# Kernel optimization log

Measured on AMD Instinct MI355X. Metric: run time of the kernel, lower is better.

## Reference

```python
import jax, jax.numpy as jnp
import numpy as np

B, T, D, H, F = 8, 1024, 512, 8, 2048
DK = D // H
EPS = 1e-3  # Keras LayerNormalization default epsilon
NEG = -1e9


def layer_norm(x, g, b):
    mu = jnp.mean(x, axis=-1, keepdims=True)
    var = jnp.mean(jnp.square(x - mu), axis=-1, keepdims=True)
    return (x - mu) * jax.lax.rsqrt(var + EPS) * g + b


def setup_inputs() -> dict:
    key = jax.random.key(0)
    ks = jax.random.split(key, 16)
    s = 1.0 / np.sqrt(D)
    sf = 1.0 / np.sqrt(F)
    x = jax.random.normal(ks[0], (B, T, D), dtype=jnp.float32)
    # binary attention mask (1 = attend). Random block-sparse-ish pattern.
    mask = (jax.random.uniform(ks[1], (B, 1, T, T)) > 0.15).astype(jnp.float32)
    return {
        "x": x,
        "mask": mask,
        "ln_in_g": jnp.ones((D,), jnp.float32),
        "ln_in_b": jnp.zeros((D,), jnp.float32),
        "Wq": jax.random.normal(ks[2], (D, D), jnp.float32) * s,
        "bq": jnp.zeros((D,), jnp.float32),
        "Wk": jax.random.normal(ks[3], (D, D), jnp.float32) * s,
        "bk": jnp.zeros((D,), jnp.float32),
        "Wv": jax.random.normal(ks[4], (D, D), jnp.float32) * s,
        "bv": jnp.zeros((D,), jnp.float32),
        "ln1_g": jnp.ones((D,), jnp.float32),
        "ln1_b": jnp.zeros((D,), jnp.float32),
        "W1": jax.random.normal(ks[5], (D, F), jnp.float32) * s,
        "b1": jnp.zeros((F,), jnp.float32),
        "W2": jax.random.normal(ks[6], (F, D), jnp.float32) * sf,
        "b2": jnp.zeros((D,), jnp.float32),
        "ln2_g": jnp.ones((D,), jnp.float32),
        "ln2_b": jnp.zeros((D,), jnp.float32),
    }


def reference(x, mask, ln_in_g, ln_in_b, Wq, bq, Wk, bk, Wv, bv,
              ln1_g, ln1_b, W1, b1, W2, b2, ln2_g, ln2_b):
    bs = x.shape[0]
    h = layer_norm(x, ln_in_g, ln_in_b)                      # [B,T,D]
    # QKV projections, split heads -> [B,H,T,DK]
    q = (h @ Wq + bq).reshape(bs, -1, H, DK).transpose(0, 2, 1, 3)
    k = (h @ Wk + bk).reshape(bs, -1, H, DK).transpose(0, 2, 1, 3)
    v = (h @ Wv + bv).reshape(bs, -1, H, DK).transpose(0, 2, 1, 3)
    scores = jnp.einsum('bhtd,bhsd->bhts', q, k) / np.sqrt(DK)
    scores = scores + NEG * (1.0 - mask)                     # additive mask
    probs = jax.nn.softmax(scores, axis=-1)                  # dropout: identity at inference
    attn = jnp.einsum('bhts,bhsd->bhtd', probs, v)
    attn = attn.transpose(0, 2, 1, 3).reshape(bs, -1, H * DK)
    # residual with ORIGINAL inputs (pre-ln_in), as in call() -> attend(inputs,...)
    attn = attn + x
    a = layer_norm(attn, ln1_g, ln1_b)
    f = jax.nn.relu(a @ W1 + b1) @ W2 + b2
    out = layer_norm(f + a, ln2_g, ln2_b)
    return out
```

## Files before the change

### kernel.cpp

```cpp
#include <hip/hip_runtime.h>

typedef unsigned short u16;
typedef unsigned long long u64;
typedef __bf16 bf16x8 __attribute__((ext_vector_type(8)));
typedef float f32x4 __attribute__((ext_vector_type(4)));

#define B_ 8
#define T_ 1024
#define D_ 512
#define H_ 8
#define DK_ 64
#define F_ 2048

__device__ __forceinline__ u16 f2bf(float f) {
    unsigned u = __float_as_uint(f);
    u += 0x7fffu + ((u >> 16) & 1u);
    return (u16)(u >> 16);
}
__device__ __forceinline__ float bf2f(u16 v) {
    return __uint_as_float((unsigned)v << 16);
}

__device__ __forceinline__ void tile_transcvt(
    const float* __restrict__ W, u16* __restrict__ WT, int K, int N, int k0, int n0,
    u16 (*t)[72])
{
    const int tid = threadIdx.x;
    const int r = tid >> 2, c4 = (tid & 3) * 16;
    const float* src = W + (size_t)(k0 + r) * N + n0 + c4;
#pragma unroll
    for (int j = 0; j < 16; j += 4) {
        float4 v = *(const float4*)(src + j);
        t[r][c4 + j]     = f2bf(v.x);
        t[r][c4 + j + 1] = f2bf(v.y);
        t[r][c4 + j + 2] = f2bf(v.z);
        t[r][c4 + j + 3] = f2bf(v.w);
    }
    __syncthreads();
    u16 tmp[16];
#pragma unroll
    for (int j = 0; j < 16; ++j) tmp[j] = t[c4 + j][r];
    u16* dst = WT + (size_t)(n0 + r) * K + k0 + c4;
    *(uint4*)dst       = *(uint4*)&tmp[0];
    *(uint4*)(dst + 8) = *(uint4*)&tmp[8];
}

__global__ __launch_bounds__(256) void prep_all(
    const float* __restrict__ Wq, const float* __restrict__ Wk, const float* __restrict__ Wv,
    const float* __restrict__ bq, const float* __restrict__ bk, const float* __restrict__ bv,
    const float* __restrict__ W1, const float* __restrict__ W2,
    const float* __restrict__ mask,
    u16* __restrict__ WqkvT, u16* __restrict__ W1T, u16* __restrict__ W2T,
    float* __restrict__ bias, u64* __restrict__ Mb)
{
    __shared__ u16 t[64][72];
    const int blk = blockIdx.x;
    const int tid = threadIdx.x;
    if (blk < 192) {
        const int k0 = (blk & 7) * 64;
        const int n0 = (blk >> 3) * 64;
        const float* W = (n0 < 512) ? Wq : (n0 < 1024 ? Wk : Wv);
        if (k0 == 0 && tid < 64) {
            int n = n0 + tid;
            bias[n] = (n < 512) ? bq[n] : (n < 1024 ? bk[n - 512] : bv[n - 1024]);
        }
        const int r = tid >> 2, c4 = (tid & 3) * 16;
        const float* src = W + (size_t)(k0 + r) * 512 + (n0 & 511) + c4;
#pragma unroll
        for (int j = 0; j < 16; j += 4) {
            float4 v = *(const float4*)(src + j);
            t[r][c4 + j]     = f2bf(v.x);
            t[r][c4 + j + 1] = f2bf(v.y);
            t[r][c4 + j + 2] = f2bf(v.z);
            t[r][c4 + j + 3] = f2bf(v.w);
        }
        __syncthreads();
        u16 tmp[16];
#pragma unroll
        for (int j = 0; j < 16; ++j) tmp[j] = t[c4 + j][r];
        u16* dst = WqkvT + (size_t)(n0 + r) * 512 + k0 + c4;
        *(uint4*)dst       = *(uint4*)&tmp[0];
        *(uint4*)(dst + 8) = *(uint4*)&tmp[8];
    } else if (blk < 448) {
        const int idx = blk - 192;
        tile_transcvt(W1, W1T, 512, 2048, (idx & 7) * 64, (idx >> 3) * 64, t);
    } else if (blk < 704) {
        const int idx = blk - 448;
        tile_transcvt(W2, W2T, 2048, 512, (idx & 31) * 64, (idx >> 5) * 64, t);
    } else {
        const int idx = blk - 704;
        int gw = (idx * 256 + tid) >> 6;
        int lane = tid & 63;
#pragma unroll
        for (int i = 0; i < 16; ++i) {
            size_t chunk = (size_t)gw * 16 + i;
            float v = mask[chunk * 64 + lane];
            u64 bm = __ballot(v > 0.5f);
            if (lane == 0) Mb[chunk] = bm;
        }
    }
}

template<int XBF, int RBF, int OB, int OF, int FILL>
__global__ __launch_bounds__(256) void ln_t(
    const void* __restrict__ Xv, const void* __restrict__ Rv,
    const float* __restrict__ g, const float* __restrict__ bt,
    u16* __restrict__ ob, float* __restrict__ of,
    const float* __restrict__ fillsrc, float* __restrict__ filldst)
{
    int wave = threadIdx.x >> 6, lane = threadIdx.x & 63;
    int row = blockIdx.x * 4 + wave;
    size_t base = (size_t)row * D_ + lane * 8;
    int c0 = lane * 8;
    float v[8];
    if (XBF) {
        const u16* X = (const u16*)Xv;
        uint4 a = *(const uint4*)(X + base);
        u16 tu[8]; *(uint4*)tu = a;
#pragma unroll
        for (int j = 0; j < 8; ++j) v[j] = bf2f(tu[j]);
    } else {
        const float* X = (const float*)Xv;
        float4 a0 = *(const float4*)(X + base);
        float4 a1 = *(const float4*)(X + base + 4);
        v[0]=a0.x; v[1]=a0.y; v[2]=a0.z; v[3]=a0.w;
        v[4]=a1.x; v[5]=a1.y; v[6]=a1.z; v[7]=a1.w;
    }
    if (Rv) {
        if (RBF) {
            const u16* R = (const u16*)Rv;
            uint4 a = *(const uint4*)(R + base);
            u16 tu[8]; *(uint4*)tu = a;
#pragma unroll
            for (int j = 0; j < 8; ++j) v[j] += bf2f(tu[j]);
        } else {
            const float* R = (const float*)Rv;
            float4 r0 = *(const float4*)(R + base);
            float4 r1 = *(const float4*)(R + base + 4);
            v[0]+=r0.x; v[1]+=r0.y; v[2]+=r0.z; v[3]+=r0.w;
            v[4]+=r1.x; v[5]+=r1.y; v[6]+=r1.z; v[7]+=r1.w;
        }
    }
    if (FILL) {
        float4 f0 = *(const float4*)(fillsrc + c0);
        float4 f1v = *(const float4*)(fillsrc + c0 + 4);
        *(float4*)(filldst + base) = f0;
        *(float4*)(filldst + base + 4) = f1v;
    }
    float s = 0.f, q = 0.f;
#pragma unroll
    for (int j = 0; j < 8; ++j) { s += v[j]; q += v[j] * v[j]; }
#pragma unroll
    for (int off = 32; off > 0; off >>= 1) {
        s += __shfl_xor(s, off);
        q += __shfl_xor(q, off);
    }
    float mu = s * (1.0f / D_);
    float var = q * (1.0f / D_) - mu * mu;
    float rstd = rsqrtf(var + 1e-3f);
    float y[8];
#pragma unroll
    for (int j = 0; j < 8; ++j) y[j] = (v[j] - mu) * rstd * g[c0 + j] + bt[c0 + j];
    if (OB) {
        u16 t[8];
#pragma unroll
        for (int j = 0; j < 8; ++j) t[j] = f2bf(y[j]);
        *(uint4*)(ob + base) = *(uint4*)t;
    }
    if (OF) {
        float4 o0, o1;
        o0.x=y[0]; o0.y=y[1]; o0.z=y[2]; o0.w=y[3];
        o1.x=y[4]; o1.y=y[5]; o1.z=y[6]; o1.w=y[7];
        *(float4*)(of + base) = o0;
        *(float4*)(of + base + 4) = o1;
    }
}

template<int BN, int RELU, int OUT>
__global__ __launch_bounds__(256) void gemm_db(
    const u16* __restrict__ A, const u16* __restrict__ BT,
    const float* __restrict__ bias, u16* __restrict__ Cb,
    float* __restrict__ Cf, int N, int K, int KS)
{
    constexpr int NI = BN / 32;
    __shared__ u16 As[2][128 * 32];
    __shared__ u16 Bs[2][BN * 32];
    const int nb = gridDim.x;
    const int flat = blockIdx.y * nb + blockIdx.x;
    const int xcd = flat & 7;
    const int idx = flat >> 3;
    const int nblk = idx >> 3;
    const int mblk = xcd * 8 + (idx & 7);
    const int tid = threadIdx.x;
    const int wave = tid >> 6, lane = tid & 63;
    const int quad = lane >> 4, l16 = lane & 15;
    const int wr = wave >> 1, wc = wave & 1;
    const int rowBase = mblk * 128;
    const int colBase = nblk * BN;
    const int lr = lane >> 2;
    const int lc = (lane & 3) * 8;
    const int kOff = blockIdx.z * KS;
    const u16* Abase = A  + (size_t)(rowBase + lr) * K + kOff + lc;
    const u16* Bbase = BT + (size_t)(colBase + lr) * K + kOff + lc;

    auto stage = [&](int k0, int buf) {
#pragma unroll
        for (int c = 0; c < 2; ++c) {
            int chunk = wave * 2 + c;
            const u16* gp = Abase + (size_t)(chunk * 16) * K + k0;
            __builtin_amdgcn_global_load_lds(
                (const __attribute__((address_space(1))) unsigned int*)gp,
                (__attribute__((address_space(3))) unsigned int*)&As[buf][chunk * 512],
                16, 0, 0);
        }
#pragma unroll
        for (int c = 0; c < BN / 64; ++c) {
            int chunk = wave * (BN / 64) + c;
            const u16* gp = Bbase + (size_t)(chunk * 16) * K + k0;
            __builtin_amdgcn_global_load_lds(
                (const __attribute__((address_space(1))) unsigned int*)gp,
                (__attribute__((address_space(3))) unsigned int*)&Bs[buf][chunk * 512],
                16, 0, 0);
        }
    };

    f32x4 acc[4][NI] = {};
    stage(0, 0);
    for (int k0 = 0; k0 < KS; k0 += 32) {
        const int buf = (k0 >> 5) & 1;
        __syncthreads();
        if (k0 + 32 < KS) stage(k0 + 32, buf ^ 1);
        bf16x8 af[4], bfr[NI];
#pragma unroll
        for (int i = 0; i < 4; ++i)
            af[i] = *(const bf16x8*)&As[buf][(wr * 64 + i * 16 + l16) * 32 + quad * 8];
#pragma unroll
        for (int j = 0; j < NI; ++j)
            bfr[j] = *(const bf16x8*)&Bs[buf][(wc * (BN / 2) + j * 16 + l16) * 32 + quad * 8];
#pragma unroll
        for (int i = 0; i < 4; ++i)
#pragma unroll
            for (int j = 0; j < NI; ++j)
                acc[i][j] = __builtin_amdgcn_mfma_f32_16x16x32_bf16(af[i], bfr[j], acc[i][j], 0, 0, 0);
    }
#pragma unroll
    for (int i = 0; i < 4; ++i) {
        int row0 = rowBase + wr * 64 + i * 16 + quad * 4;
#pragma unroll
        for (int j = 0; j < NI; ++j) {
            int col = colBase + wc * (BN / 2) + j * 16 + l16;
            float bv = (OUT == 2) ? 0.0f : bias[col];
#pragma unroll
            for (int r = 0; r < 4; ++r) {
                float v = acc[i][j][r] + bv;
                if (RELU) v = fmaxf(v, 0.0f);
                if (OUT == 2)      atomicAdd(&Cf[(size_t)(row0 + r) * N + col], v);
                else if (OUT == 1) Cb[(size_t)(row0 + r) * N + col] = f2bf(v);
                else               Cf[(size_t)(row0 + r) * N + col] = v;
            }
        }
    }
}

__global__ __launch_bounds__(256) void vtrans(const u16* __restrict__ QKV, u16* __restrict__ Vt)
{
    int blk = blockIdx.x;
    int bh = blk >> 4;
    int t0 = (blk & 15) * 64;
    int b = bh >> 3, h = bh & 7;
    __shared__ u16 tile[64][72];
    int tid = threadIdx.x;
    int r = tid >> 2;
    int c = (tid & 3) * 16;
    const u16* src = QKV + ((size_t)(b * T_) + t0 + r) * (3 * D_) + 2 * D_ + h * DK_ + c;
    *(uint4*)&tile[r][c]     = *(const uint4*)(src);
    *(uint4*)&tile[r][c + 8] = *(const uint4*)(src + 8);
    __syncthreads();
    u16 tmp[16];
#pragma unroll
    for (int j = 0; j < 16; ++j) tmp[j] = tile[c + j][r];
    u16* dst = Vt + ((size_t)bh * DK_ + r) * T_ + t0 + c;
    *(uint4*)dst       = *(uint4*)&tmp[0];
    *(uint4*)(dst + 8) = *(uint4*)&tmp[8];
}

#define APAD 72
__global__ __launch_bounds__(256) void attn_kernel(
    const u16* __restrict__ QKV, const u16* __restrict__ Vt,
    const u64* __restrict__ Mb, u16* __restrict__ Out)
{
    const int flat = blockIdx.x + 16 * (blockIdx.y + 8 * blockIdx.z);
    const int xcd = flat & 7, slot = flat >> 3;
    const int bh = xcd * 8 + (slot >> 4);
    const int qt = slot & 15;
    const int b = bh >> 3, h = bh & 7;
    const int qBase = qt * 64;
    const int tid = threadIdx.x;
    const int wave = tid >> 6, lane = tid & 63;
    const int quad = lane >> 4, l16 = lane & 15;
    __shared__ u16 Ks[64][APAD];
    __shared__ u16 Vs[64][APAD];
    __shared__ u16 Ps[4][16][APAD];

    const int qRow = qBase + wave * 16 + l16;
    const u16* qptr = QKV + ((size_t)(b * T_) + qRow) * (3 * D_) + h * DK_;
    bf16x8 qf0 = *(const bf16x8*)(qptr + quad * 8);
    bf16x8 qf1 = *(const bf16x8*)(qptr + 32 + quad * 8);

    float l_i[4] = {0.f, 0.f, 0.f, 0.f};
    f32x4 o[4] = {{0,0,0,0},{0,0,0,0},{0,0,0,0},{0,0,0,0}};

    const int sr = tid >> 2;
    const int sc = (tid & 3) * 8;
    const u16* Kg = QKV + (size_t)(b * T_) * (3 * D_) + D_ + h * DK_;
    const u16* Vg = Vt + (size_t)(b * H_ + h) * DK_ * T_;
    const u64* Mg = Mb + ((size_t)(b * T_) + qBase + wave * 16 + quad * 4) * (T_ / 64);

    uint4 kb0 = *(const uint4*)(Kg + (size_t)sr * (3 * D_) + sc);
    uint4 kb1 = *(const uint4*)(Kg + (size_t)sr * (3 * D_) + sc + 32);
    uint4 vb0 = *(const uint4*)(Vg + (size_t)sr * T_ + sc);
    uint4 vb1 = *(const uint4*)(Vg + (size_t)sr * T_ + sc + 32);

    for (int s0 = 0; s0 < T_; s0 += 64) {
        __syncthreads();
        *(uint4*)&Ks[sr][sc]      = kb0;
        *(uint4*)&Ks[sr][sc + 32] = kb1;
        *(uint4*)&Vs[sr][sc]      = vb0;
        *(uint4*)&Vs[sr][sc + 32] = vb1;
        __syncthreads();
        if (s0 + 64 < T_) {
            int s1 = s0 + 64;
            kb0 = *(const uint4*)(Kg + (size_t)(s1 + sr) * (3 * D_) + sc);
            kb1 = *(const uint4*)(Kg + (size_t)(s1 + sr) * (3 * D_) + sc + 32);
            vb0 = *(const uint4*)(Vg + (size_t)sr * T_ + s1 + sc);
            vb1 = *(const uint4*)(Vg + (size_t)sr * T_ + s1 + sc + 32);
        }

        u64 m64[4];
#pragma unroll
        for (int r = 0; r < 4; ++r) m64[r] = Mg[(size_t)r * (T_ / 64) + (s0 >> 6)];

#pragma unroll
        for (int n = 0; n < 4; ++n) {
            f32x4 s4 = {0.f, 0.f, 0.f, 0.f};
            bf16x8 kf0 = *(const bf16x8*)&Ks[n * 16 + l16][quad * 8];
            bf16x8 kf1 = *(const bf16x8*)&Ks[n * 16 + l16][32 + quad * 8];
            s4 = __builtin_amdgcn_mfma_f32_16x16x32_bf16(qf0, kf0, s4, 0, 0, 0);
            s4 = __builtin_amdgcn_mfma_f32_16x16x32_bf16(qf1, kf1, s4, 0, 0, 0);
#pragma unroll
            for (int r = 0; r < 4; ++r) {
                float p = __expf(fmaf(s4[r], 0.125f, -10.0f));
                p = ((m64[r] >> (n * 16 + l16)) & 1ull) ? p : 0.0f;
                l_i[r] += p;
                Ps[wave][quad * 4 + r][n * 16 + l16] = f2bf(p);
            }
        }
        bf16x8 pf0 = *(const bf16x8*)&Ps[wave][l16][quad * 8];
        bf16x8 pf1 = *(const bf16x8*)&Ps[wave][l16][32 + quad * 8];
#pragma unroll
        for (int dt = 0; dt < 4; ++dt) {
            bf16x8 vf0 = *(const bf16x8*)&Vs[dt * 16 + l16][quad * 8];
            bf16x8 vf1 = *(const bf16x8*)&Vs[dt * 16 + l16][32 + quad * 8];
            o[dt] = __builtin_amdgcn_mfma_f32_16x16x32_bf16(pf0, vf0, o[dt], 0, 0, 0);
            o[dt] = __builtin_amdgcn_mfma_f32_16x16x32_bf16(pf1, vf1, o[dt], 0, 0, 0);
        }
    }
#pragma unroll
    for (int off = 1; off < 16; off <<= 1) {
#pragma unroll
        for (int r = 0; r < 4; ++r) l_i[r] += __shfl_xor(l_i[r], off);
    }
    float inv[4];
#pragma unroll
    for (int r = 0; r < 4; ++r) inv[r] = 1.0f / l_i[r];
    const int orow = qBase + wave * 16 + quad * 4;
    u16* Ob = Out + ((size_t)(b * T_) + orow) * D_ + h * DK_;
#pragma unroll
    for (int dt = 0; dt < 4; ++dt) {
#pragma unroll
        for (int r = 0; r < 4; ++r)
            Ob[(size_t)r * D_ + dt * 16 + l16] = f2bf(o[dt][r] * inv[r]);
    }
}

extern "C" void kernel_launch(void* const* d_in, const int* in_sizes, int n_in,
                              void* d_out, int out_size, void* d_ws, size_t ws_size,
                              hipStream_t stream)
{
    const float* x       = (const float*)d_in[0];
    const float* mask    = (const float*)d_in[1];
    const float* ln_in_g = (const float*)d_in[2];
    const float* ln_in_b = (const float*)d_in[3];
    const float* Wq      = (const float*)d_in[4];
    const float* bq      = (const float*)d_in[5];
    const float* Wk      = (const float*)d_in[6];
    const float* bk      = (const float*)d_in[7];
    const float* Wv      = (const float*)d_in[8];
    const float* bv      = (const float*)d_in[9];
    const float* ln1_g   = (const float*)d_in[10];
    const float* ln1_b   = (const float*)d_in[11];
    const float* W1      = (const float*)d_in[12];
    const float* b1      = (const float*)d_in[13];
    const float* W2      = (const float*)d_in[14];
    const float* b2      = (const float*)d_in[15];
    const float* ln2_g   = (const float*)d_in[16];
    const float* ln2_b   = (const float*)d_in[17];
    float* out = (float*)d_out;

    char* ws = (char*)d_ws;
    size_t off = 0;
    auto alloc = [&](size_t bytes) -> void* {
        void* p = ws + off;
        off = (off + bytes + 255) & ~(size_t)255;
        return p;
    };
    u16*   WqkvT   = (u16*)alloc((size_t)1536 * 512 * 2);
    u16*   W1T     = (u16*)alloc((size_t)2048 * 512 * 2);
    u16*   W2T     = (u16*)alloc((size_t)512 * 2048 * 2);
    float* bias_q  = (float*)alloc(1536 * 4);
    u64*   Mb      = (u64*)alloc((size_t)B_ * T_ * (T_ / 64) * 8);
    u16*   h_bf    = (u16*)alloc((size_t)8192 * 512 * 2);
    u16*   QKV     = (u16*)alloc((size_t)8192 * 1536 * 2);
    u16*   Vt      = (u16*)alloc((size_t)B_ * H_ * DK_ * T_ * 2);
    u16*   attn_bf = (u16*)alloc((size_t)8192 * 512 * 2);
    u16*   a_bf    = (u16*)alloc((size_t)8192 * 512 * 2);
    u16*   f1      = (u16*)alloc((size_t)8192 * 2048 * 2);
    float* f2      = (float*)alloc((size_t)8192 * 512 * 4);
    if (off > ws_size) return;

    prep_all<<<2752, 256, 0, stream>>>(Wq, Wk, Wv, bq, bk, bv, W1, W2, mask,
                                       WqkvT, W1T, W2T, bias_q, Mb);

    ln_t<0, 0, 1, 0, 0><<<2048, 256, 0, stream>>>(
        x, nullptr, ln_in_g, ln_in_b, h_bf, nullptr, nullptr, nullptr);

    gemm_db<128, 0, 1><<<dim3(12, 64, 1), 256, 0, stream>>>(
        h_bf, WqkvT, bias_q, QKV, nullptr, 1536, 512, 512);

    vtrans<<<1024, 256, 0, stream>>>(QKV, Vt);

    attn_kernel<<<dim3(16, 8, 8), 256, 0, stream>>>(QKV, Vt, Mb, attn_bf);

    ln_t<1, 0, 1, 0, 1><<<2048, 256, 0, stream>>>(
        attn_bf, x, ln1_g, ln1_b, a_bf, nullptr, b2, f2);

    gemm_db<128, 1, 1><<<dim3(16, 64, 1), 256, 0, stream>>>(
        a_bf, W1T, b1, f1, nullptr, 2048, 512, 512);

    gemm_db<64, 0, 2><<<dim3(8, 64, 2), 256, 0, stream>>>(
        f1, W2T, nullptr, nullptr, f2, 512, 2048, 1024);

    ln_t<0, 1, 0, 1, 0><<<2048, 256, 0, stream>>>(
        f2, a_bf, ln2_g, ln2_b, nullptr, out, nullptr, nullptr);
}
```

Measured before the change: 296.9 us.

## Shrink GEMM M-tile to 64 rows and drop split-K atomics for W2 GEMM

The GEMM kernel now uses 64-row M tiles instead of 128, doubling the number of blocks for every projection and FFN GEMM. The second FFN GEMM no longer splits K across two blocks with atomicAdd into a bias-prefilled buffer. It writes f32 output directly with the bias added in the epilogue, so the LayerNorm fill of f2 is removed. This trades per-block data reuse (more global/LDS traffic per FLOP) for more parallelism and no atomics or prefill pass.

```diff
diff --git a/kernel.cpp b/kernel.cpp
--- a/kernel.cpp
+++ b/kernel.cpp
@@ -101,12 +101,11 @@
     }
 }
 
-template<int XBF, int RBF, int OB, int OF, int FILL>
+template<int XBF, int RBF, int OB, int OF>
 __global__ __launch_bounds__(256) void ln_t(
     const void* __restrict__ Xv, const void* __restrict__ Rv,
     const float* __restrict__ g, const float* __restrict__ bt,
-    u16* __restrict__ ob, float* __restrict__ of,
-    const float* __restrict__ fillsrc, float* __restrict__ filldst)
+    u16* __restrict__ ob, float* __restrict__ of)
 {
     int wave = threadIdx.x >> 6, lane = threadIdx.x & 63;
     int row = blockIdx.x * 4 + wave;
@@ -141,12 +140,6 @@
             v[4]+=r1.x; v[5]+=r1.y; v[6]+=r1.z; v[7]+=r1.w;
         }
     }
-    if (FILL) {
-        float4 f0 = *(const float4*)(fillsrc + c0);
-        float4 f1v = *(const float4*)(fillsrc + c0 + 4);
-        *(float4*)(filldst + base) = f0;
-        *(float4*)(filldst + base + 4) = f1v;
-    }
     float s = 0.f, q = 0.f;
 #pragma unroll
     for (int j = 0; j < 8; ++j) { s += v[j]; q += v[j] * v[j]; }
@@ -177,40 +170,37 @@
 }
 
 template<int BN, int RELU, int OUT>
-__global__ __launch_bounds__(256) void gemm_db(
+__global__ __launch_bounds__(256) void gemm64(
     const u16* __restrict__ A, const u16* __restrict__ BT,
     const float* __restrict__ bias, u16* __restrict__ Cb,
-    float* __restrict__ Cf, int N, int K, int KS)
+    float* __restrict__ Cf, int N, int K)
 {
     constexpr int NI = BN / 32;
-    __shared__ u16 As[2][128 * 32];
+    __shared__ u16 As[2][64 * 32];
     __shared__ u16 Bs[2][BN * 32];
     const int nb = gridDim.x;
     const int flat = blockIdx.y * nb + blockIdx.x;
     const int xcd = flat & 7;
     const int idx = flat >> 3;
-    const int nblk = idx >> 3;
-    const int mblk = xcd * 8 + (idx & 7);
+    const int nblk = idx >> 4;
+    const int mblk = xcd * 16 + (idx & 15);
     const int tid = threadIdx.x;
     const int wave = tid >> 6, lane = tid & 63;
     const int quad = lane >> 4, l16 = lane & 15;
     const int wr = wave >> 1, wc = wave & 1;
-    const int rowBase = mblk * 128;
+    const int rowBase = mblk * 64;
     const int colBase = nblk * BN;
     const int lr = lane >> 2;
     const int lc = (lane & 3) * 8;
-    const int kOff = blockIdx.z * KS;
-    const u16* Abase = A  + (size_t)(rowBase + lr) * K + kOff + lc;
-    const u16* Bbase = BT + (size_t)(colBase + lr) * K + kOff + lc;
+    const u16* Abase = A  + (size_t)(rowBase + lr) * K + lc;
+    const u16* Bbase = BT + (size_t)(colBase + lr) * K + lc;
 
     auto stage = [&](int k0, int buf) {
-#pragma unroll
-        for (int c = 0; c < 2; ++c) {
-            int chunk = wave * 2 + c;
-            const u16* gp = Abase + (size_t)(chunk * 16) * K + k0;
+        {
+            const u16* gp = Abase + (size_t)(wave * 16) * K + k0;
             __builtin_amdgcn_global_load_lds(
                 (const __attribute__((address_space(1))) unsigned int*)gp,
-                (__attribute__((address_space(3))) unsigned int*)&As[buf][chunk * 512],
+                (__attribute__((address_space(3))) unsigned int*)&As[buf][wave * 512],
                 16, 0, 0);
         }
 #pragma unroll
@@ -224,39 +214,38 @@
         }
     };
 
-    f32x4 acc[4][NI] = {};
+    f32x4 acc[2][NI] = {};
     stage(0, 0);
-    for (int k0 = 0; k0 < KS; k0 += 32) {
+    for (int k0 = 0; k0 < K; k0 += 32) {
         const int buf = (k0 >> 5) & 1;
         __syncthreads();
-        if (k0 + 32 < KS) stage(k0 + 32, buf ^ 1);
-        bf16x8 af[4], bfr[NI];
-#pragma unroll
-        for (int i = 0; i < 4; ++i)
-            af[i] = *(const bf16x8*)&As[buf][(wr * 64 + i * 16 + l16) * 32 + quad * 8];
+        if (k0 + 32 < K) stage(k0 + 32, buf ^ 1);
+        bf16x8 af[2], bfr[NI];
+#pragma unroll
+        for (int i = 0; i < 2; ++i)
+            af[i] = *(const bf16x8*)&As[buf][(wr * 32 + i * 16 + l16) * 32 + quad * 8];
 #pragma unroll
         for (int j = 0; j < NI; ++j)
             bfr[j] = *(const bf16x8*)&Bs[buf][(wc * (BN / 2) + j * 16 + l16) * 32 + quad * 8];
 #pragma unroll
-        for (int i = 0; i < 4; ++i)
+        for (int i = 0; i < 2; ++i)
 #pragma unroll
             for (int j = 0; j < NI; ++j)
                 acc[i][j] = __builtin_amdgcn_mfma_f32_16x16x32_bf16(af[i], bfr[j], acc[i][j], 0, 0, 0);
     }
 #pragma unroll
-    for (int i = 0; i < 4; ++i) {
-        int row0 = rowBase + wr * 64 + i * 16 + quad * 4;
+    for (int i = 0; i < 2; ++i) {
+        int row0 = rowBase + wr * 32 + i * 16 + quad * 4;
 #pragma unroll
         for (int j = 0; j < NI; ++j) {
             int col = colBase + wc * (BN / 2) + j * 16 + l16;
-            float bv = (OUT == 2) ? 0.0f : bias[col];
+            float bv = bias[col];
 #pragma unroll
             for (int r = 0; r < 4; ++r) {
                 float v = acc[i][j][r] + bv;
                 if (RELU) v = fmaxf(v, 0.0f);
-                if (OUT == 2)      atomicAdd(&Cf[(size_t)(row0 + r) * N + col], v);
-                else if (OUT == 1) Cb[(size_t)(row0 + r) * N + col] = f2bf(v);
-                else               Cf[(size_t)(row0 + r) * N + col] = v;
+                if (OUT == 1) Cb[(size_t)(row0 + r) * N + col] = f2bf(v);
+                else          Cf[(size_t)(row0 + r) * N + col] = v;
             }
         }
     }
@@ -431,25 +420,25 @@
     prep_all<<<2752, 256, 0, stream>>>(Wq, Wk, Wv, bq, bk, bv, W1, W2, mask,
                                        WqkvT, W1T, W2T, bias_q, Mb);
 
-    ln_t<0, 0, 1, 0, 0><<<2048, 256, 0, stream>>>(
-        x, nullptr, ln_in_g, ln_in_b, h_bf, nullptr, nullptr, nullptr);
-
-    gemm_db<128, 0, 1><<<dim3(12, 64, 1), 256, 0, stream>>>(
-        h_bf, WqkvT, bias_q, QKV, nullptr, 1536, 512, 512);
+    ln_t<0, 0, 1, 0><<<2048, 256, 0, stream>>>(
+        x, nullptr, ln_in_g, ln_in_b, h_bf, nullptr);
+
+    gemm64<128, 0, 1><<<dim3(12, 128), 256, 0, stream>>>(
+        h_bf, WqkvT, bias_q, QKV, nullptr, 1536, 512);
 
     vtrans<<<1024, 256, 0, stream>>>(QKV, Vt);
 
     attn_kernel<<<dim3(16, 8, 8), 256, 0, stream>>>(QKV, Vt, Mb, attn_bf);
 
-    ln_t<1, 0, 1, 0, 1><<<2048, 256, 0, stream>>>(
-        attn_bf, x, ln1_g, ln1_b, a_bf, nullptr, b2, f2);
-
-    gemm_db<128, 1, 1><<<dim3(16, 64, 1), 256, 0, stream>>>(
-        a_bf, W1T, b1, f1, nullptr, 2048, 512, 512);
-
-    gemm_db<64, 0, 2><<<dim3(8, 64, 2), 256, 0, stream>>>(
-        f1, W2T, nullptr, nullptr, f2, 512, 2048, 1024);
-
-    ln_t<0, 1, 0, 1, 0><<<2048, 256, 0, stream>>>(
-        f2, a_bf, ln2_g, ln2_b, nullptr, out, nullptr, nullptr);
-}
+    ln_t<1, 0, 1, 0><<<2048, 256, 0, stream>>>(
+        attn_bf, x, ln1_g, ln1_b, a_bf, nullptr);
+
+    gemm64<128, 1, 1><<<dim3(16, 128), 256, 0, stream>>>(
+        a_bf, W1T, b1, f1, nullptr, 2048, 512);
+
+    gemm64<64, 0, 0><<<dim3(8, 128), 256, 0, stream>>>(
+        f1, W2T, b2, nullptr, f2, 512, 2048);
+
+    ln_t<0, 1, 0, 1><<<2048, 256, 0, stream>>>(
+        f2, a_bf, ln2_g, ln2_b, nullptr, out);
+}
```

New measurement: 288.0 us. -3.0%, faster.
